# Performance work log

Measured on AMD Instinct MI355X. Metric: run time of the kernel, lower is better.

Reference implementation:

```python
import jax, jax.numpy as jnp
import numpy as np

B, S, D = 4, 2048, 1024
HALF_PI = np.float32(np.pi / 2.0)


def setup_inputs() -> dict:
    key = jax.random.key(0)
    ks = jax.random.split(key, 12)
    std = np.float32(0.02)
    def w(k):
        return jax.random.normal(k, (D, D), dtype=jnp.float32) * std
    return {
        "x": jax.random.normal(ks[0], (B, S, D), dtype=jnp.float32),
        "W_q": w(ks[1]), "b_q": jnp.zeros((D,), jnp.float32),
        "W_k": w(ks[2]), "b_k": jnp.zeros((D,), jnp.float32),
        "W_v": w(ks[3]), "b_v": jnp.zeros((D,), jnp.float32),
        "W_t": w(ks[4]), "b_t": jnp.zeros((D,), jnp.float32),
        "W_o": w(ks[5]), "b_o": jnp.zeros((D,), jnp.float32),
        "entangle_strength": jnp.float32(0.5),
    }


def reference(x, W_q, b_q, W_k, b_k, W_v, b_v, W_t, b_t, W_o, b_o, entangle_strength):
    scale = jnp.float32(np.sqrt(D))
    Q = x @ W_q + b_q          # [B,S,D]
    K = x @ W_k + b_k
    V = x @ W_v + b_v
    # theta in [0, pi/2]; r = cos(2*theta)
    theta_q = jax.nn.sigmoid(Q @ W_t + b_t) * HALF_PI
    theta_k = jax.nn.sigmoid(K @ W_t + b_t) * HALF_PI
    r_q = jnp.cos(2.0 * theta_q)
    r_k = jnp.cos(2.0 * theta_k)
    classical = jnp.einsum("bqd,bkd->bqk", Q, K) / scale
    quantum = jnp.einsum("bqd,bkd->bqk", r_q, r_k) * entangle_strength
    attn_weights = jax.nn.softmax(classical + quantum, axis=-1)  # [B,S,S]
    # dropout: eval mode -> identity
    out = jnp.einsum("bqk,bkd->bqd", attn_weights, V)
    out = out @ W_o + b_o
    return out, attn_weights
```

## Files before the change

kernel.cpp:

```cpp
#include <hip/hip_runtime.h>
#include <cstdint>

typedef unsigned short u16;
typedef __attribute__((ext_vector_type(8))) short bf16x8;
typedef __attribute__((ext_vector_type(16))) float f32x16;

__device__ __forceinline__ u16 f2b(float x) {
  unsigned u = __float_as_uint(x);
  u += 0x7FFFu + ((u >> 16) & 1u);
  return (u16)(u >> 16);
}

__device__ __forceinline__ void gload16(const void* g, void* l) {
  __builtin_amdgcn_global_load_lds(
      (const __attribute__((address_space(1))) void*)g,
      (__attribute__((address_space(3))) void*)l, 16, 0, 0);
}

__device__ __forceinline__ void vmwait0() {
  asm volatile("s_waitcnt vmcnt(0)" ::: "memory");
}

template <int L>
__device__ __forceinline__ void stage_half(const u16* __restrict__ G,
                                           long long ld, int kb,
                                           u16* Ldst, int tid) {
#pragma unroll
  for (int j = 0; j < L; ++j) {
    const int P = j * 512 + tid;
    const int r = P >> 3, c = P & 7;
    gload16(G + (long long)r * ld + kb + ((c ^ (r & 7)) << 3), Ldst + P * 8);
  }
}

__device__ __forceinline__ bf16x8 fr8(const u16* R, int row, int chunk) {
  return *(const bf16x8*)(R + row * 64 + ((chunk ^ (row & 7)) << 3));
}

template <int EPI, int NF>
__global__ __launch_bounds__(512, 2) void g32(
    const u16* __restrict__ A, long long lda, long long sAz,
    const u16* __restrict__ B, long long ldb, long long sBz,
    void* __restrict__ C0, void* __restrict__ C1, void* __restrict__ C2,
    long long ldc, long long sCz, int K,
    const float* __restrict__ b0, const float* __restrict__ b1,
    const float* __restrict__ b2, float preScale, const float* __restrict__ esp) {
  constexpr int BN = NF * 128;
  constexpr int AH = 8192;
  constexpr int BH = NF * 4096;
  constexpr int BUFU = 2 * AH + 2 * BH;
  __shared__ __align__(16) u16 lds[2 * BUFU];

  const int gx = gridDim.x, S = gx * gridDim.y;
  const int hw = blockIdx.y * gx + blockIdx.x;
  const int l = (hw & 7) * (S >> 3) + (hw >> 3);
  const int bx = l % gx, by = l / gx;
  const int z = blockIdx.z;
  const long long tM = (long long)by * 256;
  const long long tN = (long long)bx * BN;
  const u16* GA = A + z * sAz + tM * lda;
  const u16* GB = B + z * sBz + tN * ldb;
  const int tid = threadIdx.x;
  const int NT = K >> 6;

  stage_half<4>(GA, lda, 0, lds, tid);
  stage_half<2 * NF>(GB, ldb, 0, lds + 2 * AH, tid);
  vmwait0();
  __builtin_amdgcn_s_barrier();

  const int wid = tid >> 6, lane = tid & 63;
  const int wm = wid >> 2, wn = wid & 3;
  const int l31 = lane & 31, hk = lane >> 5;
  f32x16 acc[4][NF] = {};

  for (int t = 0; t < NT; ++t) {
    u16* cur = lds + (t & 1) * BUFU;
    u16* oth = lds + ((t + 1) & 1) * BUFU;
    if (t + 1 < NT) {
      stage_half<4>(GA, lda, (t + 1) * 64, oth, tid);
      stage_half<2 * NF>(GB, ldb, (t + 1) * 64, oth + 2 * AH, tid);
    }
    const u16* Ahp = cur + wm * AH;
    const u16* Bhp = cur + 2 * AH + (wn >> 1) * BH;
    const int bbase = (wn & 1) * NF * 32;
    bf16x8 a[4][2], b[NF][2];
#pragma unroll
    for (int kp = 0; kp < 2; ++kp) {
#pragma unroll
      for (int mf = 0; mf < 4; ++mf) {
        a[mf][0] = fr8(Ahp, mf * 32 + l31, 4 * kp + hk);
        a[mf][1] = fr8(Ahp, mf * 32 + l31, 4 * kp + 2 + hk);
      }
#pragma unroll
      for (int nf = 0; nf < NF; ++nf) {
        b[nf][0] = fr8(Bhp, bbase + nf * 32 + l31, 4 * kp + hk);
        b[nf][1] = fr8(Bhp, bbase + nf * 32 + l31, 4 * kp + 2 + hk);
      }
      __builtin_amdgcn_s_setprio(1);
#pragma unroll
      for (int s = 0; s < 2; ++s)
#pragma unroll
        for (int mf = 0; mf < 4; ++mf)
#pragma unroll
          for (int nf = 0; nf < NF; ++nf)
            acc[mf][nf] = __builtin_amdgcn_mfma_f32_32x32x16_bf16(
                a[mf][s], b[nf][s], acc[mf][nf], 0, 0, 0);
      __builtin_amdgcn_s_setprio(0);
    }
    if (t + 1 < NT) vmwait0();
    __builtin_amdgcn_s_barrier();
  }

  float ps = preScale, mul = 1.0f;
  if constexpr (EPI == 1) {
    ps = (z == 0) ? preScale : 1.0f;
    mul = (z == 0) ? esp[0] : 1.0f;
  }
#pragma unroll
  for (int mf = 0; mf < 4; ++mf) {
#pragma unroll
    for (int nf = 0; nf < NF; ++nf) {
      const int col = (int)tN + wn * NF * 32 + nf * 32 + l31;
      const f32x16 vv = acc[mf][nf];
#pragma unroll
      for (int reg = 0; reg < 16; ++reg) {
        const long long row =
            tM + wm * 128 + mf * 32 + (reg & 3) + 8 * (reg >> 2) + 4 * hk;
        const float v = vv[reg];
        if constexpr (EPI == 0) {
          const int gg = col >> 10, cc = col & 1023;
          if (gg == 0)      ((u16*)C0)[row * 2048 + cc] = f2b((v + b0[cc]) * 0.03125f);
          else if (gg == 1) ((u16*)C1)[row * 2048 + cc] = f2b(v + b1[cc]);
          else              ((u16*)C2)[row * 1024 + cc] = f2b(v + b2[cc]);
        } else if constexpr (EPI == 1) {
          const float tt = v * ps + b0[col];
          const float sg = 1.f / (1.f + __expf(-tt));
          ((u16*)C0)[z * sCz + row * ldc + col] = f2b(mul * cospif(sg));
        } else if constexpr (EPI == 2) {
          ((u16*)C0)[z * sCz + row * ldc + col] = f2b(v);
        } else if constexpr (EPI == 3) {
          ((float*)C0)[z * sCz + row * ldc + col] = v + b0[col];
        } else {
          ((float*)C0)[z * sCz + row * ldc + col] = v;
        }
      }
    }
  }
}

__global__ __launch_bounds__(256) void softmax_rows(float* __restrict__ L,
                                                    u16* __restrict__ AB) {
  const long long row = blockIdx.x;
  float4* p4 = (float4*)(L + row * 2048);
  const int tid = threadIdx.x;
  float4 a = p4[tid], b = p4[tid + 256];
  float m = fmaxf(fmaxf(fmaxf(a.x, a.y), fmaxf(a.z, a.w)),
                  fmaxf(fmaxf(b.x, b.y), fmaxf(b.z, b.w)));
#pragma unroll
  for (int o = 32; o > 0; o >>= 1) m = fmaxf(m, __shfl_xor(m, o));
  __shared__ float rmax[4], rsum[4];
  const int wid = tid >> 6, lane = tid & 63;
  if (lane == 0) rmax[wid] = m;
  __syncthreads();
  m = fmaxf(fmaxf(rmax[0], rmax[1]), fmaxf(rmax[2], rmax[3]));
  a.x = __expf(a.x - m); a.y = __expf(a.y - m);
  a.z = __expf(a.z - m); a.w = __expf(a.w - m);
  b.x = __expf(b.x - m); b.y = __expf(b.y - m);
  b.z = __expf(b.z - m); b.w = __expf(b.w - m);
  float s = a.x + a.y + a.z + a.w + b.x + b.y + b.z + b.w;
#pragma unroll
  for (int o = 32; o > 0; o >>= 1) s += __shfl_xor(s, o);
  if (lane == 0) rsum[wid] = s;
  __syncthreads();
  s = rsum[0] + rsum[1] + rsum[2] + rsum[3];
  const float inv = 1.0f / s;
  a.x *= inv; a.y *= inv; a.z *= inv; a.w *= inv;
  b.x *= inv; b.y *= inv; b.z *= inv; b.w *= inv;
  p4[tid] = a;
  p4[tid + 256] = b;
  ushort4* o4 = (ushort4*)(AB + row * 2048);
  o4[tid]       = make_ushort4(f2b(a.x), f2b(a.y), f2b(a.z), f2b(a.w));
  o4[tid + 256] = make_ushort4(f2b(b.x), f2b(b.y), f2b(b.z), f2b(b.w));
}

__global__ __launch_bounds__(256) void cvt_x(const float* __restrict__ X,
                                             u16* __restrict__ XB) {
  const int i = blockIdx.x * 256 + threadIdx.x;
  float4 v = ((const float4*)X)[i];
  ((ushort4*)XB)[i] = make_ushort4(f2b(v.x), f2b(v.y), f2b(v.z), f2b(v.w));
}

__global__ void cvt_w(const float* __restrict__ W0, const float* __restrict__ W1,
                      const float* __restrict__ W2, const float* __restrict__ W3,
                      const float* __restrict__ W4, u16* __restrict__ WT) {
  __shared__ float t[32][33];
  const int z = blockIdx.z;
  const float* W = (z == 0) ? W0 : (z == 1) ? W1 : (z == 2) ? W2 : (z == 3) ? W3 : W4;
  u16* D = WT + (long long)z * 1024 * 1024;
  const int c0 = blockIdx.x * 32, r0 = blockIdx.y * 32;
  const int tx = threadIdx.x, ty = threadIdx.y;
#pragma unroll
  for (int i = 0; i < 4; ++i)
    t[ty + i * 8][tx] = W[(long long)(r0 + ty + i * 8) * 1024 + c0 + tx];
  __syncthreads();
#pragma unroll
  for (int i = 0; i < 4; ++i)
    D[(long long)(c0 + ty + i * 8) * 1024 + r0 + tx] = f2b(t[tx][ty + i * 8]);
}

__global__ void transpose_v(const u16* __restrict__ Vb, u16* __restrict__ VT) {
  __shared__ u16 t[32][33];
  const int b = blockIdx.z;
  const u16* V = Vb + (long long)b * 2048 * 1024;
  u16* O = VT + (long long)b * 1024 * 2048;
  const int d0 = blockIdx.x * 32, s0 = blockIdx.y * 32;
  const int tx = threadIdx.x, ty = threadIdx.y;
#pragma unroll
  for (int i = 0; i < 4; ++i)
    t[ty + i * 8][tx] = V[(long long)(s0 + ty + i * 8) * 1024 + d0 + tx];
  __syncthreads();
#pragma unroll
  for (int i = 0; i < 4; ++i)
    O[(long long)(d0 + ty + i * 8) * 2048 + s0 + tx] = t[tx][ty + i * 8];
}

extern "C" void kernel_launch(void* const* d_in, const int* in_sizes, int n_in,
                              void* d_out, int out_size, void* d_ws,
                              size_t ws_size, hipStream_t stream) {
  const float* x  = (const float*)d_in[0];
  const float* Wq = (const float*)d_in[1];
  const float* bq = (const float*)d_in[2];
  const float* Wk = (const float*)d_in[3];
  const float* bk = (const float*)d_in[4];
  const float* Wv = (const float*)d_in[5];
  const float* bv = (const float*)d_in[6];
  const float* Wt = (const float*)d_in[7];
  const float* bt = (const float*)d_in[8];
  const float* Wo = (const float*)d_in[9];
  const float* bo = (const float*)d_in[10];
  const float* es = (const float*)d_in[11];

  char* ws = (char*)d_ws;
  u16* WT   = (u16*)(ws);
  u16* XB   = (u16*)(ws + 10485760);
  u16* Qcat = (u16*)(ws + 27262976);
  u16* Kcat = Qcat + 16777216;
  u16* Vb   = (u16*)(ws + 94371840);
  u16* VT   = (u16*)(ws + 111149056);
  u16* WtT  = WT + 3 * 1048576;
  u16* WoT  = WT + 4 * 1048576;
  u16* ATT  = Qcat;
  u16* AV   = XB;

  float* outO = (float*)d_out;
  float* outA = outO + 8388608;

  cvt_x<<<8192, 256, 0, stream>>>(x, XB);
  cvt_w<<<dim3(32, 32, 5), dim3(32, 8), 0, stream>>>(Wq, Wk, Wv, Wt, Wo, WT);
  g32<0, 1><<<dim3(24, 32, 1), 512, 0, stream>>>(
      XB, 1024, 0, WT, 1024, 0, Qcat, Kcat, Vb, 0, 0, 1024, bq, bk, bv,
      1.f, nullptr);
  g32<1, 2><<<dim3(4, 32, 2), 512, 0, stream>>>(
      Qcat, 2048, 16777216LL, WtT, 1024, 0, Qcat + 1024, nullptr, nullptr,
      2048, 16777216LL, 1024, bt, nullptr, nullptr, 32.f, es);
  transpose_v<<<dim3(32, 64, 4), dim3(32, 8), 0, stream>>>(Vb, VT);
  g32<4, 2><<<dim3(8, 8, 4), 512, 0, stream>>>(
      Qcat, 2048, 4194304LL, Kcat, 2048, 4194304LL, outA, nullptr, nullptr,
      2048, 4194304LL, 2048, nullptr, nullptr, nullptr, 1.f, nullptr);
  softmax_rows<<<8192, 256, 0, stream>>>(outA, ATT);
  g32<2, 1><<<dim3(8, 8, 4), 512, 0, stream>>>(
      ATT, 2048, 4194304LL, VT, 2048, 2097152LL, AV, nullptr, nullptr,
      1024, 2097152LL, 2048, nullptr, nullptr, nullptr, 1.f, nullptr);
  g32<3, 1><<<dim3(8, 32, 1), 512, 0, stream>>>(
      AV, 1024, 0, WoT, 1024, 0, outO, nullptr, nullptr,
      1024, 0, 1024, bo, nullptr, nullptr, 1.f, nullptr);
}
```

Before: 355.7 us.

## Replace GEMM kernel with 128x128 tile, 3-stage LDS pipeline using 16x16 MFMA

Replaces the 256-row, 512-thread double-buffered GEMM that used 32x32x16 MFMA with a 256-thread kernel using 128x128 tiles and BK=32. Loads run through a three-buffer LDS ring with partial vmcnt waits, so global loads for two steps ahead overlap compute. The inner product now uses 16x16x32 MFMA. Smaller tiles give more blocks per launch and higher occupancy, at the cost of lower arithmetic intensity and more LDS fragment reads per FLOP.

```diff
diff --git a/kernel.cpp b/kernel.cpp
--- a/kernel.cpp
+++ b/kernel.cpp
@@ -3,7 +3,7 @@
 
 typedef unsigned short u16;
 typedef __attribute__((ext_vector_type(8))) short bf16x8;
-typedef __attribute__((ext_vector_type(16))) float f32x16;
+typedef __attribute__((ext_vector_type(4))) float f32x4;
 
 __device__ __forceinline__ u16 f2b(float x) {
   unsigned u = __float_as_uint(x);
@@ -17,116 +17,103 @@
       (__attribute__((address_space(3))) void*)l, 16, 0, 0);
 }
 
-__device__ __forceinline__ void vmwait0() {
-  asm volatile("s_waitcnt vmcnt(0)" ::: "memory");
-}
-
-template <int L>
-__device__ __forceinline__ void stage_half(const u16* __restrict__ G,
-                                           long long ld, int kb,
-                                           u16* Ldst, int tid) {
-#pragma unroll
-  for (int j = 0; j < L; ++j) {
-    const int P = j * 512 + tid;
-    const int r = P >> 3, c = P & 7;
-    gload16(G + (long long)r * ld + kb + ((c ^ (r & 7)) << 3), Ldst + P * 8);
-  }
-}
-
-__device__ __forceinline__ bf16x8 fr8(const u16* R, int row, int chunk) {
-  return *(const bf16x8*)(R + row * 64 + ((chunk ^ (row & 7)) << 3));
-}
-
-template <int EPI, int NF>
-__global__ __launch_bounds__(512, 2) void g32(
+template <int N>
+__device__ __forceinline__ void vmwait() {
+  if constexpr (N == 0) asm volatile("s_waitcnt vmcnt(0)" ::: "memory");
+  else if constexpr (N == 4) asm volatile("s_waitcnt vmcnt(4)" ::: "memory");
+  else if constexpr (N == 8) asm volatile("s_waitcnt vmcnt(8)" ::: "memory");
+}
+
+__device__ __forceinline__ void stage128(const u16* __restrict__ G,
+                                         long long ld, int kb,
+                                         u16* Ldst, int tid) {
+#pragma unroll
+  for (int j = 0; j < 2; ++j) {
+    const int P = j * 256 + tid;
+    const int vr = P >> 3;
+    const int ch = (P & 7) ^ (vr & 7);
+    const int r = vr * 2 + (ch >> 2), c = ch & 3;
+    gload16(G + (long long)r * ld + kb + c * 8, Ldst + P * 8);
+  }
+}
+
+__device__ __forceinline__ bf16x8 fr4(const u16* R, int row, int chunk) {
+  const int vr = row >> 1;
+  const int ch = (((row & 1) << 2) | chunk) ^ (vr & 7);
+  return *(const bf16x8*)(R + vr * 64 + ch * 8);
+}
+
+template <int EPI>
+__global__ __launch_bounds__(256, 3) void e3p(
     const u16* __restrict__ A, long long lda, long long sAz,
     const u16* __restrict__ B, long long ldb, long long sBz,
     void* __restrict__ C0, void* __restrict__ C1, void* __restrict__ C2,
     long long ldc, long long sCz, int K,
     const float* __restrict__ b0, const float* __restrict__ b1,
     const float* __restrict__ b2, float preScale, const float* __restrict__ esp) {
-  constexpr int BN = NF * 128;
-  constexpr int AH = 8192;
-  constexpr int BH = NF * 4096;
-  constexpr int BUFU = 2 * AH + 2 * BH;
-  __shared__ __align__(16) u16 lds[2 * BUFU];
+  constexpr int HALF = 4096;
+  constexpr int BUFU = 2 * HALF;
+  __shared__ __align__(16) u16 lds[3 * BUFU];
 
   const int gx = gridDim.x, S = gx * gridDim.y;
   const int hw = blockIdx.y * gx + blockIdx.x;
   const int l = (hw & 7) * (S >> 3) + (hw >> 3);
   const int bx = l % gx, by = l / gx;
   const int z = blockIdx.z;
-  const long long tM = (long long)by * 256;
-  const long long tN = (long long)bx * BN;
+  const long long tM = (long long)by * 128;
+  const long long tN = (long long)bx * 128;
   const u16* GA = A + z * sAz + tM * lda;
   const u16* GB = B + z * sBz + tN * ldb;
   const int tid = threadIdx.x;
-  const int NT = K >> 6;
-
-  stage_half<4>(GA, lda, 0, lds, tid);
-  stage_half<2 * NF>(GB, ldb, 0, lds + 2 * AH, tid);
-  vmwait0();
-  __builtin_amdgcn_s_barrier();
+  const int NT = K >> 5;
+
+  stage128(GA, lda, 0, lds, tid);
+  stage128(GB, ldb, 0, lds + HALF, tid);
+  stage128(GA, lda, 32, lds + BUFU, tid);
+  stage128(GB, ldb, 32, lds + BUFU + HALF, tid);
 
   const int wid = tid >> 6, lane = tid & 63;
-  const int wm = wid >> 2, wn = wid & 3;
-  const int l31 = lane & 31, hk = lane >> 5;
-  f32x16 acc[4][NF] = {};
+  const int wr = (wid >> 1) * 64, wc = (wid & 1) * 64;
+  const int lr = lane & 15, cA = lane >> 4;
+  f32x4 acc[4][4] = {};
 
   for (int t = 0; t < NT; ++t) {
-    u16* cur = lds + (t & 1) * BUFU;
-    u16* oth = lds + ((t + 1) & 1) * BUFU;
-    if (t + 1 < NT) {
-      stage_half<4>(GA, lda, (t + 1) * 64, oth, tid);
-      stage_half<2 * NF>(GB, ldb, (t + 1) * 64, oth + 2 * AH, tid);
+    if (t < NT - 1) vmwait<4>(); else vmwait<0>();
+    __builtin_amdgcn_s_barrier();
+    if (t + 2 < NT) {
+      u16* nxt = lds + ((t + 2) % 3) * BUFU;
+      stage128(GA, lda, (t + 2) * 32, nxt, tid);
+      stage128(GB, ldb, (t + 2) * 32, nxt + HALF, tid);
     }
-    const u16* Ahp = cur + wm * AH;
-    const u16* Bhp = cur + 2 * AH + (wn >> 1) * BH;
-    const int bbase = (wn & 1) * NF * 32;
-    bf16x8 a[4][2], b[NF][2];
-#pragma unroll
-    for (int kp = 0; kp < 2; ++kp) {
-#pragma unroll
-      for (int mf = 0; mf < 4; ++mf) {
-        a[mf][0] = fr8(Ahp, mf * 32 + l31, 4 * kp + hk);
-        a[mf][1] = fr8(Ahp, mf * 32 + l31, 4 * kp + 2 + hk);
-      }
-#pragma unroll
-      for (int nf = 0; nf < NF; ++nf) {
-        b[nf][0] = fr8(Bhp, bbase + nf * 32 + l31, 4 * kp + hk);
-        b[nf][1] = fr8(Bhp, bbase + nf * 32 + l31, 4 * kp + 2 + hk);
-      }
-      __builtin_amdgcn_s_setprio(1);
-#pragma unroll
-      for (int s = 0; s < 2; ++s)
-#pragma unroll
-        for (int mf = 0; mf < 4; ++mf)
-#pragma unroll
-          for (int nf = 0; nf < NF; ++nf)
-            acc[mf][nf] = __builtin_amdgcn_mfma_f32_32x32x16_bf16(
-                a[mf][s], b[nf][s], acc[mf][nf], 0, 0, 0);
-      __builtin_amdgcn_s_setprio(0);
-    }
-    if (t + 1 < NT) vmwait0();
-    __builtin_amdgcn_s_barrier();
-  }
-
+    const u16* cur = lds + (t % 3) * BUFU;
+    bf16x8 a[4], b[4];
+#pragma unroll
+    for (int m = 0; m < 4; ++m) a[m] = fr4(cur, wr + m * 16 + lr, cA);
+#pragma unroll
+    for (int n = 0; n < 4; ++n) b[n] = fr4(cur + HALF, wc + n * 16 + lr, cA);
+#pragma unroll
+    for (int m = 0; m < 4; ++m)
+#pragma unroll
+      for (int n = 0; n < 4; ++n)
+        acc[m][n] = __builtin_amdgcn_mfma_f32_16x16x32_bf16(a[m], b[n],
+                                                            acc[m][n], 0, 0, 0);
+  }
+
+  const int rr = (lane >> 4) << 2;
   float ps = preScale, mul = 1.0f;
   if constexpr (EPI == 1) {
     ps = (z == 0) ? preScale : 1.0f;
     mul = (z == 0) ? esp[0] : 1.0f;
   }
 #pragma unroll
-  for (int mf = 0; mf < 4; ++mf) {
-#pragma unroll
-    for (int nf = 0; nf < NF; ++nf) {
-      const int col = (int)tN + wn * NF * 32 + nf * 32 + l31;
-      const f32x16 vv = acc[mf][nf];
-#pragma unroll
-      for (int reg = 0; reg < 16; ++reg) {
-        const long long row =
-            tM + wm * 128 + mf * 32 + (reg & 3) + 8 * (reg >> 2) + 4 * hk;
-        const float v = vv[reg];
+  for (int m = 0; m < 4; ++m) {
+#pragma unroll
+    for (int n = 0; n < 4; ++n) {
+      const int col = (int)tN + wc + n * 16 + lr;
+#pragma unroll
+      for (int r = 0; r < 4; ++r) {
+        const long long row = tM + wr + m * 16 + rr + r;
+        const float v = acc[m][n][r];
         if constexpr (EPI == 0) {
           const int gg = col >> 10, cc = col & 1023;
           if (gg == 0)      ((u16*)C0)[row * 2048 + cc] = f2b((v + b0[cc]) * 0.03125f);
@@ -257,21 +244,21 @@
 
   cvt_x<<<8192, 256, 0, stream>>>(x, XB);
   cvt_w<<<dim3(32, 32, 5), dim3(32, 8), 0, stream>>>(Wq, Wk, Wv, Wt, Wo, WT);
-  g32<0, 1><<<dim3(24, 32, 1), 512, 0, stream>>>(
+  e3p<0><<<dim3(24, 64, 1), 256, 0, stream>>>(
       XB, 1024, 0, WT, 1024, 0, Qcat, Kcat, Vb, 0, 0, 1024, bq, bk, bv,
       1.f, nullptr);
-  g32<1, 2><<<dim3(4, 32, 2), 512, 0, stream>>>(
+  e3p<1><<<dim3(8, 64, 2), 256, 0, stream>>>(
       Qcat, 2048, 16777216LL, WtT, 1024, 0, Qcat + 1024, nullptr, nullptr,
       2048, 16777216LL, 1024, bt, nullptr, nullptr, 32.f, es);
   transpose_v<<<dim3(32, 64, 4), dim3(32, 8), 0, stream>>>(Vb, VT);
-  g32<4, 2><<<dim3(8, 8, 4), 512, 0, stream>>>(
+  e3p<4><<<dim3(16, 16, 4), 256, 0, stream>>>(
       Qcat, 2048, 4194304LL, Kcat, 2048, 4194304LL, outA, nullptr, nullptr,
       2048, 4194304LL, 2048, nullptr, nullptr, nullptr, 1.f, nullptr);
   softmax_rows<<<8192, 256, 0, stream>>>(outA, ATT);
-  g32<2, 1><<<dim3(8, 8, 4), 512, 0, stream>>>(
+  e3p<2><<<dim3(8, 16, 4), 256, 0, stream>>>(
       ATT, 2048, 4194304LL, VT, 2048, 2097152LL, AV, nullptr, nullptr,
       1024, 2097152LL, 2048, nullptr, nullptr, nullptr, 1.f, nullptr);
-  g32<3, 1><<<dim3(8, 32, 1), 512, 0, stream>>>(
+  e3p<3><<<dim3(8, 64, 1), 256, 0, stream>>>(
       AV, 1024, 0, WoT, 1024, 0, outO, nullptr, nullptr,
       1024, 0, 1024, bo, nullptr, nullptr, 1.f, nullptr);
 }
```

New measurement: 352.1 us. No clear change (-1.0%).
